# Performance work log

Measured on AMD Instinct MI355X. Metric: run time of the kernel, lower is better.

## Reference

```python
import jax, jax.numpy as jnp
import numpy as np
import math

N, E, T, H, IN_DIM, G, L = 8192, 131072, 262144, 128, 64, 32, 2
RBF_BINS, RBF_MAX, ANG_BINS = 32, 5.0, 16


def _rbf(d, r_max, n_bins):
    centers = jnp.linspace(0.0, r_max, n_bins, dtype=jnp.float32)
    delta = r_max / max(n_bins - 1, 1)
    gamma = 1.0 / (2.0 * (delta ** 2 + 1e-12))
    diff = d[:, None] - centers[None, :]
    return jnp.exp(-gamma * diff * diff)


def _mlp2(x, w1, b1, w2, b2):
    return jax.nn.silu(x @ w1 + b1) @ w2 + b2


def _ln(x, g, b):
    mu = jnp.mean(x, -1, keepdims=True)
    var = jnp.mean((x - mu) ** 2, -1, keepdims=True)
    return (x - mu) * jax.lax.rsqrt(var + 1e-5) * g + b


def _safe_norm(v):
    # ||v|| with grad-safe sqrt at v=0
    return jnp.sqrt(jnp.sum(v * v, -1) + 1e-12)


def setup_inputs() -> dict:
    key = jax.random.key(0)
    ks = iter(jax.random.split(key, 64))

    def lin(fan_in, shape):
        return jax.random.normal(next(ks), shape, jnp.float32) * (fan_in ** -0.5)

    x = jax.random.normal(next(ks), (N, IN_DIM), jnp.float32)
    pos = jax.random.normal(next(ks), (N, 3), jnp.float32) * 2.0
    edge_index = jax.random.randint(next(ks), (2, E), 0, N, jnp.int32)
    edge_dist = jnp.linalg.norm(pos[edge_index[1]] - pos[edge_index[0]], axis=-1)
    triplet_kj = jax.random.randint(next(ks), (T,), 0, E, jnp.int32)
    triplet_ji = jax.random.randint(next(ks), (T,), 0, E, jnp.int32)
    batch = jnp.sort(jax.random.randint(next(ks), (N,), 0, G, jnp.int32))
    TM_IN, MM_IN, CTX = 2 * RBF_BINS + ANG_BINS, 3 * H + RBF_BINS, 3 * H
    d = dict(
        x=x, pos=pos, edge_dist=edge_dist,
        node_in_w=lin(IN_DIM, (IN_DIM, H)), node_in_b=jnp.zeros(H),
        tm_w1=lin(TM_IN, (L, TM_IN, H)), tm_b1=jnp.zeros((L, H)),
        tm_w2=lin(H, (L, H, H)), tm_b2=jnp.zeros((L, H)),
        mm_w1=lin(MM_IN, (L, MM_IN, H)), mm_b1=jnp.zeros((L, H)),
        mm_w2=lin(H, (L, H, 2 * H)), mm_b2=jnp.zeros((L, 2 * H)),
        us_w1=lin(CTX, (L, CTX, H)), us_b1=jnp.zeros((L, H)),
        us_w2=lin(H, (L, H, H)), us_b2=jnp.zeros((L, H)),
        gv_w1=lin(CTX, (L, CTX, H)), gv_b1=jnp.zeros((L, H)),
        gv_w2=lin(H, (L, H, H)), gv_b2=jnp.zeros((L, H)),
        ln_g=jnp.ones((L, H)), ln_b=jnp.zeros((L, H)),
        vn_init=jnp.zeros(H),
        v2n_w1=lin(H, (H, H)), v2n_b1=jnp.zeros(H),
        v2n_w2=lin(H, (H, H)), v2n_b2=jnp.zeros(H),
        n2v_w1=lin(H, (H, H)), n2v_b1=jnp.zeros(H),
        n2v_w2=lin(H, (H, H)), n2v_b2=jnp.zeros(H),
        head_w1=lin(5 * H, (5 * H, H)), head_b1=jnp.zeros(H),
        head_w2=lin(H, (H, 1)), head_b2=jnp.zeros(1),
        edge_index=edge_index, triplet_kj=triplet_kj,
        triplet_ji=triplet_ji, batch=batch,
    )
    return d


def reference(x, pos, edge_dist, node_in_w, node_in_b, tm_w1, tm_b1, tm_w2, tm_b2,
              mm_w1, mm_b1, mm_w2, mm_b2, us_w1, us_b1, us_w2, us_b2,
              gv_w1, gv_b1, gv_w2, gv_b2, ln_g, ln_b, vn_init,
              v2n_w1, v2n_b1, v2n_w2, v2n_b2, n2v_w1, n2v_b1, n2v_w2, n2v_b2,
              head_w1, head_b1, head_w2, head_b2,
              edge_index, triplet_kj, triplet_ji, batch):
    src, dst = edge_index[0], edge_index[1]
    s = x @ node_in_w + node_in_b                              # [N,H]
    v = jnp.zeros((N, H, 3), s.dtype)                          # [N,H,3]
    vec = pos[dst] - pos[src]                                  # [E,3]
    edge_dir = vec / (edge_dist[:, None] + 1e-9)               # [E,3]
    edge_rbf = _rbf(edge_dist, RBF_MAX, RBF_BINS)              # [E,32]
    # 3-body angles between edge ji and edge kj
    a, b = vec[triplet_ji], vec[triplet_kj]                    # [T,3]
    cos = jnp.sum(a * b, -1) / (_safe_norm(a) * _safe_norm(b) + 1e-9)
    angle = jnp.arccos(jnp.clip(cos, -1.0 + 1e-7, 1.0 - 1e-7))
    angle_feat = _rbf(angle, math.pi, ANG_BINS)                # [T,16]
    vn = jnp.broadcast_to(vn_init, (G, H))
    for l in range(L):
        s = s + _mlp2(vn, v2n_w1, v2n_b1, v2n_w2, v2n_b2)[batch]
        # triplet gather -> MLP -> scatter onto edges
        t_in = jnp.concatenate([edge_rbf[triplet_kj], edge_rbf[triplet_ji], angle_feat], -1)
        t_msg = _mlp2(t_in, tm_w1[l], tm_b1[l], tm_w2[l], tm_b2[l])
        angle_agg = jax.ops.segment_sum(t_msg, triplet_ji, num_segments=E)   # [E,H]
        # edge messages -> scatter onto nodes (scalar + vector channels)
        msg_in = jnp.concatenate([s[src], s[dst], edge_rbf, angle_agg], -1)  # [E,416]
        msg = _mlp2(msg_in, mm_w1[l], mm_b1[l], mm_w2[l], mm_b2[l])          # [E,2H]
        m_s, m_vc = msg[:, :H], msg[:, H:]
        agg_s = jax.ops.segment_sum(m_s, dst, num_segments=N)                # [N,H]
        m_v = m_vc[:, :, None] * edge_dir[:, None, :]                        # [E,H,3]
        agg_v = jax.ops.segment_sum(m_v.reshape(E, H * 3), dst, num_segments=N).reshape(N, H, 3)
        ctx = jnp.concatenate([s, agg_s, _safe_norm(v)], -1)                 # [N,3H]
        s = s + _mlp2(ctx, us_w1[l], us_b1[l], us_w2[l], us_b2[l])
        gate = jax.nn.sigmoid(_mlp2(ctx, gv_w1[l], gv_b1[l], gv_w2[l], gv_b2[l]))
        v = v + gate[:, :, None] * agg_v
        s = jax.nn.silu(_ln(s, ln_g[l], ln_b[l]))
        vn = vn + _mlp2(jax.ops.segment_sum(s, batch, num_segments=G),
                        n2v_w1, n2v_b1, n2v_w2, n2v_b2)
    nf = jnp.concatenate([s, _safe_norm(v)], -1)                             # [N,2H]
    add_p = jax.ops.segment_sum(nf, batch, num_segments=G)
    counts = jax.ops.segment_sum(jnp.ones((N,), nf.dtype), batch, num_segments=G)
    mean_p = add_p / jnp.maximum(counts, 1.0)[:, None]
    g = jnp.concatenate([add_p, mean_p, vn], -1)                             # [G,5H]
    pred = _mlp2(g, head_w1, head_b1, head_w2, head_b2)                      # [G,1]
    return pred[:, 0]
```

## Files before the change

kernel.cpp:

```cpp
#include <hip/hip_runtime.h>
#include <math.h>

#define N_   8192
#define E_   131072
#define T_   262144
#define H_   128
#define IND_ 64
#define G_   32
#define L_   2

#define CW 64
#define RB 16

#define MROWS 32
#define HSTRIDE 136
#define WSTRIDE 36

#define STEP_E  ((float)(5.0/31.0))
#define GAMMA_E ((float)(1.0/(2.0*((5.0/31.0)*(5.0/31.0) + 1e-12))))
#define PI_D    3.14159265358979323846
#define STEP_A  ((float)(PI_D/15.0))
#define GAMMA_A ((float)(1.0/(2.0*((PI_D/15.0)*(PI_D/15.0) + 1e-12))))

typedef __attribute__((ext_vector_type(8))) short short8;
typedef __attribute__((ext_vector_type(4))) float f32x4;
typedef unsigned short ushort_t;

static __device__ __forceinline__ float silu_f(float x){ return x / (1.f + expf(-x)); }
static __device__ __forceinline__ float sigmoid_f(float x){ return 1.f / (1.f + expf(-x)); }

static __device__ __forceinline__ ushort_t f2bf(float x){
  unsigned int u = __builtin_bit_cast(unsigned int, x);
  u += 0x7FFFu + ((u >> 16) & 1u);
  return (ushort_t)(u >> 16);
}
static __device__ __forceinline__ float bf2f(ushort_t h){
  unsigned int u = ((unsigned int)h) << 16;
  return __builtin_bit_cast(float, u);
}


__global__ void k_zero(float* __restrict__ p, long n){
  long stride = (long)gridDim.x*256;
  long n4 = n >> 2;
  float4* p4 = (float4*)p;
  for (long i = (long)blockIdx.x*256 + threadIdx.x; i < n4; i += stride)
    p4[i] = make_float4(0.f,0.f,0.f,0.f);
  for (long i = (n4<<2) + (long)blockIdx.x*256 + threadIdx.x; i < n; i += stride)
    p[i] = 0.f;
}

__global__ void k_sentinel(float* __restrict__ p, int n){
  int i = blockIdx.x*256 + threadIdx.x;
  if (i < n) p[i] = 1.0e30f;
}

__global__ void k_init_vn(float* __restrict__ vn, const float* __restrict__ vn_init){
  int i = blockIdx.x*256 + threadIdx.x;
  if (i < G_*H_) vn[i] = vn_init[i & 127];
}

__global__ void k_bhist(const int* __restrict__ batch, int* __restrict__ bh){
  int i = blockIdx.x*256 + threadIdx.x;
  if (i < N_) atomicAdd(&bh[batch[i]], 1);
}
__global__ void k_bscan(int* __restrict__ bh){
  if (threadIdx.x == 0 && blockIdx.x == 0){
    int a = 0;
    for (int g=0; g<G_; g++){ a += bh[g]; bh[g] = a; }
  }
}

__global__ void k_wt_all(const float* __restrict__ tm_w1, const float* __restrict__ tm_w2,
                         const float* __restrict__ mm_w1, const float* __restrict__ mm_w2,
                         const float* __restrict__ us_w1, const float* __restrict__ us_w2,
                         const float* __restrict__ gv_w1, const float* __restrict__ gv_w2,
                         ushort_t* __restrict__ wtbuf){
  const int l = blockIdx.y;
  int i = blockIdx.x*256 + threadIdx.x;
  if (i >= 245760) return;
  ushort_t* base = wtbuf + (size_t)l*376832;
  if (i < 12288){
    int c = i/96, k = i%96;
    base[i] = (k < 80) ? f2bf(tm_w1[(size_t)l*10240 + (size_t)k*128 + c]) : (ushort_t)0;
  } else if (i < 28672){
    int j = i - 12288; int c = j >> 7, k = j & 127;
    base[12288 + j] = f2bf(tm_w2[(size_t)l*16384 + (size_t)k*128 + c]);
  } else if (i < 81920){
    int j = i - 28672; int c = j/416, k = j%416;
    base[28672 + j] = f2bf(mm_w1[(size_t)l*53248 + (size_t)k*128 + c]);
  } else if (i < 114688){
    int j = i - 81920; int c = j >> 7, k = j & 127;
    base[81920 + j] = f2bf(mm_w2[(size_t)l*32768 + (size_t)k*256 + c]);
  } else if (i < 163840){
    int j = i - 114688; int c = j/384, k = j%384;
    float w = us_w1[(size_t)l*49152 + (size_t)k*128 + c];
    ushort_t h = f2bf(w);
    base[114688 + j] = h; base[163840 + j] = f2bf(w - bf2f(h));
  } else if (i < 180224){
    int j = i - 163840; int c = j >> 7, k = j & 127;
    float w = us_w2[(size_t)l*16384 + (size_t)k*128 + c];
    ushort_t h = f2bf(w);
    base[212992 + j] = h; base[229376 + j] = f2bf(w - bf2f(h));
  } else if (i < 229376){
    int j = i - 180224; int c = j/384, k = j%384;
    float w = gv_w1[(size_t)l*49152 + (size_t)k*128 + c];
    ushort_t h = f2bf(w);
    base[245760 + j] = h; base[294912 + j] = f2bf(w - bf2f(h));
  } else {
    int j = i - 229376; int c = j >> 7, k = j & 127;
    float w = gv_w2[(size_t)l*16384 + (size_t)k*128 + c];
    ushort_t h = f2bf(w);
    base[344064 + j] = h; base[360448 + j] = f2bf(w - bf2f(h));
  }
}

__global__ void k_geom(const float* __restrict__ pos, const float* __restrict__ dist,
                       const int* __restrict__ ei,
                       float* __restrict__ vec, float* __restrict__ dir,
                       ushort_t* __restrict__ rbf16){
  int e = blockIdx.x*256 + threadIdx.x;
  if (e >= E_) return;
  int s = ei[e], d = ei[E_ + e];
  float vx = pos[d*3+0] - pos[s*3+0];
  float vy = pos[d*3+1] - pos[s*3+1];
  float vz = pos[d*3+2] - pos[s*3+2];
  vec[e*3+0]=vx; vec[e*3+1]=vy; vec[e*3+2]=vz;
  float dd = dist[e];
  float inv = 1.f / (dd + 1e-9f);
  dir[e*3+0]=vx*inv; dir[e*3+1]=vy*inv; dir[e*3+2]=vz*inv;
  #pragma unroll
  for (int i=0;i<32;i++){
    float df = dd - i*STEP_E;
    rbf16[e*32+i] = f2bf(expf(-GAMMA_E*df*df));
  }
}

__global__ void k_dirs(const float* __restrict__ dir, const int* __restrict__ perm_e,
                       float* __restrict__ dir_s){
  int p = blockIdx.x*256 + threadIdx.x;
  if (p >= E_) return;
  int e = perm_e[p];
  dir_s[p*3+0] = dir[e*3+0];
  dir_s[p*3+1] = dir[e*3+1];
  dir_s[p*3+2] = dir[e*3+2];
}

__global__ void k_angle(const float* __restrict__ vec,
                        const int* __restrict__ kj, const int* __restrict__ ji,
                        float* __restrict__ angle){
  int t = blockIdx.x*256 + threadIdx.x;
  if (t >= T_) return;
  int ea = ji[t], eb = kj[t];
  float ax=vec[ea*3+0], ay=vec[ea*3+1], az=vec[ea*3+2];
  float bx=vec[eb*3+0], by=vec[eb*3+1], bz=vec[eb*3+2];
  float dot = ax*bx + ay*by + az*bz;
  float na = sqrtf(ax*ax+ay*ay+az*az + 1e-12f);
  float nb = sqrtf(bx*bx+by*by+bz*bz + 1e-12f);
  float c = dot / (na*nb + 1e-9f);
  c = fminf(fmaxf(c, -1.f + 1e-7f), 1.f - 1e-7f);
  angle[t] = acosf(c);
}


__global__ void k_hist(const int* __restrict__ keys, int M, int* __restrict__ hist){
  int i = blockIdx.x*256 + threadIdx.x;
  if (i < M) atomicAdd(&hist[keys[i]], 1);
}

__global__ void k_hist2(const int* __restrict__ keys, const int* __restrict__ map,
                        int M, int* __restrict__ hist){
  int i = blockIdx.x*256 + threadIdx.x;
  if (i < M) atomicAdd(&hist[map[keys[i]]], 1);
}

__global__ void k_scan1(const int* __restrict__ in, int* __restrict__ out,
                        int* __restrict__ sums, int B){
  __shared__ int sh[1024];
  int base = blockIdx.x*1024, t = threadIdx.x;
  for (int j=t;j<1024;j+=256) sh[j] = (base+j<B) ? in[base+j] : 0;
  __syncthreads();
  for (int o=1;o<1024;o<<=1){
    int v[4];
    #pragma unroll
    for (int q=0;q<4;q++){ int idx=t+q*256; v[q]=(idx>=o)? sh[idx-o]:0; }
    __syncthreads();
    #pragma unroll
    for (int q=0;q<4;q++){ int idx=t+q*256; sh[idx]+=v[q]; }
    __syncthreads();
  }
  for (int j=t;j<1024;j+=256) if (base+j<B) out[base+j] = (j==0)?0:sh[j-1];
  if (t==0) sums[blockIdx.x] = sh[1023];
}

__global__ void k_scan2(int* __restrict__ sums, int nb){
  if (threadIdx.x==0 && blockIdx.x==0){
    int a=0;
    for (int i=0;i<nb;i++){ int x=sums[i]; sums[i]=a; a+=x; }
  }
}

__global__ void k_scan3(int* __restrict__ out, const int* __restrict__ sums, int B){
  int i = blockIdx.x*256+threadIdx.x;
  if (i<B) out[i] += sums[i>>10];
}

__global__ void k_fill(const int* __restrict__ keys, int M, int* __restrict__ cur,
                       int* __restrict__ perm){
  int i = blockIdx.x*256+threadIdx.x;
  if (i<M){ int p = atomicAdd(&cur[keys[i]],1); perm[p]=i; }
}

__global__ void k_fill2(const int* __restrict__ keys, const int* __restrict__ map,
                        int M, int* __restrict__ cur, int* __restrict__ perm){
  int i = blockIdx.x*256+threadIdx.x;
  if (i<M){ int p = atomicAdd(&cur[map[keys[i]]],1); perm[p]=i; }
}

__global__ void k_invert(const int* __restrict__ perm, int* __restrict__ rank, int M){
  int i = blockIdx.x*256+threadIdx.x;
  if (i<M) rank[perm[i]] = i;
}

template<int SM, int K1PAD>
__launch_bounds__(256, 3)
__global__ void k_mlp1(
    const int* __restrict__ perm,
    const int* __restrict__ idx1, const int* __restrict__ idx2,
    const ushort_t* __restrict__ rbf16, const float* __restrict__ angle,
    const ushort_t* __restrict__ s16, const ushort_t* __restrict__ eagg_in,
    const ushort_t* __restrict__ W1t, const float* __restrict__ b1,
    ushort_t* __restrict__ outbuf)
{
  __shared__ ushort_t lw[128*WSTRIDE];
  __shared__ ushort_t hid[4*MROWS*HSTRIDE];
  const int tid  = threadIdx.x;
  const int wave = tid >> 6;
  const int lane = tid & 63;
  const int n    = lane & 15;
  const int quad = lane >> 4;
  const int kq   = quad*8;
  const int wrow = blockIdx.x*128 + wave*MROWS;
  ushort_t* myhid = hid + wave*MROWS*HSTRIDE;

  const int e0 = perm[wrow + n];
  const int e1 = perm[wrow + 16 + n];

  int i1a = idx1[e0], i1b = idx1[e1];
  int i2a = idx2[e0], i2b = idx2[e1];
  float ang0 = 0.f, ang1 = 0.f;
  if (SM == 1){ ang0 = angle[e0]; ang1 = angle[e1]; }

  f32x4 acc[2][8];
  #pragma unroll
  for (int rh=0;rh<2;rh++)
    #pragma unroll
    for (int ct=0;ct<8;ct++) acc[rh][ct] = (f32x4){0.f,0.f,0.f,0.f};

  #pragma unroll
  for (int k0 = 0; k0 < K1PAD; k0 += 32){
    #pragma unroll
    for (int it=0; it<2; it++){
      int idx = tid + it*256;
      int col = idx >> 2, seg = idx & 3;
      *(short8*)&lw[col*WSTRIDE + seg*8] = *(const short8*)&W1t[(size_t)col*K1PAD + k0 + seg*8];
    }
    __syncthreads();

    short8 a0, a1;
    if (SM == 1){
      if (k0 == 0){
        a0 = *(const short8*)&rbf16[(size_t)i1a*32 + kq];
        a1 = *(const short8*)&rbf16[(size_t)i1b*32 + kq];
      } else if (k0 == 32){
        a0 = *(const short8*)&rbf16[(size_t)i2a*32 + kq];
        a1 = *(const short8*)&rbf16[(size_t)i2b*32 + kq];
      } else {
        #pragma unroll
        for (int j=0;j<8;j++){
          int kk = kq + j;
          float v0 = 0.f, v1 = 0.f;
          if (kk < 16){
            float c = (float)kk*STEP_A;
            float d0 = ang0 - c, d1 = ang1 - c;
            v0 = expf(-GAMMA_A*d0*d0); v1 = expf(-GAMMA_A*d1*d1);
          }
          a0[j] = (short)f2bf(v0); a1[j] = (short)f2bf(v1);
        }
      }
    } else {
      const int k = k0 + kq;
      if (k0 < 128){
        a0 = *(const short8*)&s16[(size_t)i1a*128 + k];
        a1 = *(const short8*)&s16[(size_t)i1b*128 + k];
      } else if (k0 < 256){
        a0 = *(const short8*)&s16[(size_t)i2a*128 + (k-128)];
        a1 = *(const short8*)&s16[(size_t)i2b*128 + (k-128)];
      } else if (k0 < 288){
        a0 = *(const short8*)&rbf16[(size_t)e0*32 + (k-256)];
        a1 = *(const short8*)&rbf16[(size_t)e1*32 + (k-256)];
      } else {
        a0 = *(const short8*)&eagg_in[(size_t)(wrow + n)*128 + (k-288)];
        a1 = *(const short8*)&eagg_in[(size_t)(wrow + 16 + n)*128 + (k-288)];
      }
    }
    #pragma unroll
    for (int ct=0;ct<8;ct++){
      short8 b = *(const short8*)&lw[(ct*16 + n)*WSTRIDE + kq];
      acc[0][ct] = __builtin_amdgcn_mfma_f32_16x16x32_bf16(a0, b, acc[0][ct], 0,0,0);
      acc[1][ct] = __builtin_amdgcn_mfma_f32_16x16x32_bf16(a1, b, acc[1][ct], 0,0,0);
    }
    __syncthreads();
  }

  #pragma unroll
  for (int rh=0;rh<2;rh++){
    #pragma unroll
    for (int ct=0;ct<8;ct++){
      int col = ct*16 + n;
      float bv = b1[col];
      #pragma unroll
      for (int reg=0;reg<4;reg++){
        int rloc = rh*16 + quad*4 + reg;
        float h = acc[rh][ct][reg] + bv;
        myhid[rloc*HSTRIDE + col] = f2bf(silu_f(h));
      }
    }
  }
  const int rsub = lane >> 4;
  const int c8   = (lane & 15) * 8;
  #pragma unroll
  for (int i=0;i<8;i++){
    int rloc = i*4 + rsub;
    int grow = wrow + rloc;
    short8 vv = *(const short8*)&myhid[(size_t)rloc*HSTRIDE + c8];
    *(short8*)&outbuf[(size_t)grow*128 + c8] = vv;
  }
}

__launch_bounds__(64, 4)
__global__ void k_aggemm_t(const ushort_t* __restrict__ tmsg, const int* __restrict__ tends,
                           const ushort_t* __restrict__ W2t, const float* __restrict__ b2,
                           ushort_t* __restrict__ eagg2){
  __shared__ ushort_t hid[MROWS*HSTRIDE];
  const int lane = threadIdx.x;
  const int n    = lane & 15;
  const int quad = lane >> 4;
  const int kq   = quad*8;
  const int wrow = blockIdx.x*MROWS;
  const int r0 = wrow + n, r1 = wrow + 16 + n;
  const int s0 = r0 ? tends[r0-1] : 0;
  const int e0 = tends[r0];
  const int s1 = tends[r1-1];
  const int e1 = tends[r1];

  f32x4 acc[2][8];
  #pragma unroll
  for (int rh=0;rh<2;rh++)
    #pragma unroll
    for (int ct=0;ct<8;ct++) acc[rh][ct] = (f32x4){0.f,0.f,0.f,0.f};

  #pragma unroll
  for (int k0=0;k0<128;k0+=32){
    float sum0[8], sum1[8];
    #pragma unroll
    for (int j=0;j<8;j++){ sum0[j]=0.f; sum1[j]=0.f; }
    for (int p=s0;p<e0;p++){
      short8 w = *(const short8*)&tmsg[(size_t)p*128 + k0 + kq];
      #pragma unroll
      for (int j=0;j<8;j++) sum0[j] += bf2f((ushort_t)w[j]);
    }
    for (int p=s1;p<e1;p++){
      short8 w = *(const short8*)&tmsg[(size_t)p*128 + k0 + kq];
      #pragma unroll
      for (int j=0;j<8;j++) sum1[j] += bf2f((ushort_t)w[j]);
    }
    short8 a0, a1;
    #pragma unroll
    for (int j=0;j<8;j++){
      a0[j] = (short)f2bf(sum0[j]);
      a1[j] = (short)f2bf(sum1[j]);
    }
    #pragma unroll
    for (int ct=0;ct<8;ct++){
      short8 b = *(const short8*)&W2t[(size_t)(ct*16 + n)*128 + k0 + kq];
      acc[0][ct] = __builtin_amdgcn_mfma_f32_16x16x32_bf16(a0, b, acc[0][ct], 0,0,0);
      acc[1][ct] = __builtin_amdgcn_mfma_f32_16x16x32_bf16(a1, b, acc[1][ct], 0,0,0);
    }
  }

  float cnts[2][4];
  #pragma unroll
  for (int rh=0;rh<2;rh++)
    #pragma unroll
    for (int reg=0;reg<4;reg++){
      int row = wrow + rh*16 + quad*4 + reg;
      cnts[rh][reg] = (float)(tends[row] - (row ? tends[row-1] : 0));
    }

  #pragma unroll
  for (int rh=0;rh<2;rh++){
    #pragma unroll
    for (int ct=0;ct<8;ct++){
      int col = ct*16 + n;
      float bv = b2[col];
      #pragma unroll
      for (int reg=0;reg<4;reg++){
        int rloc = rh*16 + quad*4 + reg;
        hid[rloc*HSTRIDE + col] = f2bf(acc[rh][ct][reg] + cnts[rh][reg]*bv);
      }
    }
  }
  const int rsub = lane >> 4;
  const int c8   = (lane & 15) * 8;
  #pragma unroll
  for (int i=0;i<8;i++){
    int rloc = i*4 + rsub;
    int grow = wrow + rloc;
    short8 vv = *(const short8*)&hid[(size_t)rloc*HSTRIDE + c8];
    *(short8*)&eagg2[(size_t)grow*128 + c8] = vv;
  }
}

__global__ void k_agg_e(const ushort_t* __restrict__ hbuf, const int* __restrict__ eends,
                        const float* __restrict__ dir_s, float* __restrict__ mom){
  int i = blockIdx.x*256 + threadIdx.x;
  int d = i >> 6, c2 = (i & 63)*2;
  if (d >= N_) return;
  int s = (d == 0) ? 0 : eends[d-1];
  int e = eends[d];
  float hs0=0.f,hs1=0.f, hx0=0.f,hx1=0.f, hy0=0.f,hy1=0.f, hz0=0.f,hz1=0.f;
  float sdx=0.f, sdy=0.f, sdz=0.f;
  for (int q=s;q<e;q++){
    unsigned int w = *(const unsigned int*)&hbuf[(size_t)q*128 + c2];
    float h0 = bf2f((ushort_t)(w & 0xFFFFu));
    float h1 = bf2f((ushort_t)(w >> 16));
    float dx = dir_s[q*3+0], dy = dir_s[q*3+1], dz = dir_s[q*3+2];
    hs0 += h0; hs1 += h1;
    hx0 += h0*dx; hx1 += h1*dx;
    hy0 += h0*dy; hy1 += h1*dy;
    hz0 += h0*dz; hz1 += h1*dz;
    sdx += dx; sdy += dy; sdz += dz;
  }
  size_t base = (size_t)d*128 + c2;
  *(float2*)&mom[base]                        = make_float2(hs0, hs1);
  *(float2*)&mom[(size_t)N_*128   + base]     = make_float2(hx0, hx1);
  *(float2*)&mom[(size_t)N_*256   + base]     = make_float2(hy0, hy1);
  *(float2*)&mom[(size_t)N_*384   + base]     = make_float2(hz0, hz1);
  if (c2 == 0){
    mom[(size_t)N_*512 + d*4+0] = sdx;
    mom[(size_t)N_*512 + d*4+1] = sdy;
    mom[(size_t)N_*512 + d*4+2] = sdz;
  }
}

__launch_bounds__(64, 4)
__global__ void k_gemm_e(const float* __restrict__ mom, const int* __restrict__ eends,
                         const ushort_t* __restrict__ W2t ,
                         const float* __restrict__ b2 ,
                         const float* __restrict__ v ,
                         ushort_t* __restrict__ a16h, ushort_t* __restrict__ a16l,
                         ushort_t* __restrict__ vnh,  ushort_t* __restrict__ vnl,
                         float* __restrict__ aggv ){
  __shared__ float sbuf[MROWS*130];
  const int lane = threadIdx.x;
  const int n    = lane & 15;
  const int quad = lane >> 4;
  const int kq   = quad*8;
  const int wrow = blockIdx.x*MROWS;
  const int og   = blockIdx.y;

  const float* M = mom + (size_t)og*((size_t)N_*128);
  const ushort_t* W = W2t + (og ? (size_t)128*128 : 0);

  f32x4 acc[2][8];
  #pragma unroll
  for (int rh=0;rh<2;rh++)
    #pragma unroll
    for (int ct=0;ct<8;ct++) acc[rh][ct] = (f32x4){0.f,0.f,0.f,0.f};

  #pragma unroll
  for (int k0=0;k0<128;k0+=32){
    const int k = k0 + kq;
    const float* p0 = &M[(size_t)(wrow + n)*128 + k];
    const float* p1 = &M[(size_t)(wrow + 16 + n)*128 + k];
    f32x4 x0 = *(const f32x4*)p0, x1 = *(const f32x4*)(p0+4);
    f32x4 y0 = *(const f32x4*)p1, y1 = *(const f32x4*)(p1+4);
    short8 ah0, al0, ah1, al1;
    #pragma unroll
    for (int j=0;j<4;j++){
      ushort_t h;
      h = f2bf(x0[j]); ah0[j]   = (short)h; al0[j]   = (short)f2bf(x0[j] - bf2f(h));
      h = f2bf(x1[j]); ah0[4+j] = (short)h; al0[4+j] = (short)f2bf(x1[j] - bf2f(h));
      h = f2bf(y0[j]); ah1[j]   = (short)h; al1[j]   = (short)f2bf(y0[j] - bf2f(h));
      h = f2bf(y1[j]); ah1[4+j] = (short)h; al1[4+j] = (short)f2bf(y1[j] - bf2f(h));
    }
    #pragma unroll
    for (int ct=0;ct<8;ct++){
      short8 b = *(const short8*)&W[(size_t)(ct*16 + n)*128 + k0 + kq];
      acc[0][ct] = __builtin_amdgcn_mfma_f32_16x16x32_bf16(ah0, b, acc[0][ct], 0,0,0);
      acc[0][ct] = __builtin_amdgcn_mfma_f32_16x16x32_bf16(al0, b, acc[0][ct], 0,0,0);
      acc[1][ct] = __builtin_amdgcn_mfma_f32_16x16x32_bf16(ah1, b, acc[1][ct], 0,0,0);
      acc[1][ct] = __builtin_amdgcn_mfma_f32_16x16x32_bf16(al1, b, acc[1][ct], 0,0,0);
    }
  }

  const int rsub = lane >> 4;
  const int c8   = (lane & 15) * 8;

  if (og == 0){
    float cnts[2][4];
    #pragma unroll
    for (int rh=0;rh<2;rh++)
      #pragma unroll
      for (int reg=0;reg<4;reg++){
        int row = wrow + rh*16 + quad*4 + reg;
        cnts[rh][reg] = (float)(eends[row] - (row ? eends[row-1] : 0));
      }
    ushort_t* us = (ushort_t*)sbuf;
    #pragma unroll
    for (int rh=0;rh<2;rh++)
      #pragma unroll
      for (int ct=0;ct<8;ct++){
        int col = ct*16 + n;
        float bv = b2[col];
        #pragma unroll
        for (int reg=0;reg<4;reg++){
          int rloc = rh*16 + quad*4 + reg;
          float val = acc[rh][ct][reg] + cnts[rh][reg]*bv;
          us[rloc*HSTRIDE + col] = f2bf(val);
        }
      }
    #pragma unroll
    for (int i=0;i<8;i++){
      int rloc = i*4 + rsub;
      short8 vv = *(const short8*)&us[(size_t)rloc*HSTRIDE + c8];
      *(short8*)&a16h[(size_t)(wrow + rloc)*128 + c8] = vv;
    }
    #pragma unroll
    for (int rh=0;rh<2;rh++)
      #pragma unroll
      for (int ct=0;ct<8;ct++){
        int col = ct*16 + n;
        float bv = b2[col];
        #pragma unroll
        for (int reg=0;reg<4;reg++){
          int rloc = rh*16 + quad*4 + reg;
          float val = acc[rh][ct][reg] + cnts[rh][reg]*bv;
          ushort_t h = f2bf(val);
          us[rloc*HSTRIDE + col] = f2bf(val - bf2f(h));
        }
      }
    #pragma unroll
    for (int i=0;i<8;i++){
      int rloc = i*4 + rsub;
      short8 vv = *(const short8*)&us[(size_t)rloc*HSTRIDE + c8];
      *(short8*)&a16l[(size_t)(wrow + rloc)*128 + c8] = vv;
    }
    #pragma unroll 4
    for (int j=0;j<32;j++){
      size_t idx = (size_t)wrow*128 + (size_t)j*128 + lane*2;
      float2 a = *(const float2*)&v[idx];
      float2 b = *(const float2*)&v[(size_t)N_*128 + idx];
      float2 c = *(const float2*)&v[(size_t)N_*256 + idx];
      float n0 = sqrtf(a.x*a.x + b.x*b.x + c.x*c.x + 1e-12f);
      float n1 = sqrtf(a.y*a.y + b.y*b.y + c.y*c.y + 1e-12f);
      ushort_t h0 = f2bf(n0), h1 = f2bf(n1);
      *(unsigned int*)&vnh[idx] = (unsigned int)h0 | ((unsigned int)h1 << 16);
      *(unsigned int*)&vnl[idx] = (unsigned int)f2bf(n0 - bf2f(h0))
                                | ((unsigned int)f2bf(n1 - bf2f(h1)) << 16);
    }
  } else {
    const int x = og - 1;
    #pragma unroll
    for (int rh=0;rh<2;rh++)
      #pragma unroll
      for (int ct=0;ct<8;ct++){
        int col = ct*16 + n;
        float bv = b2[128 + col];
        #pragma unroll
        for (int reg=0;reg<4;reg++){
          int rloc = rh*16 + quad*4 + reg;
          int row = wrow + rloc;
          float sd = mom[(size_t)N_*512 + row*4 + x];
          sbuf[rloc*130 + col] = acc[rh][ct][reg] + sd*bv;
        }
      }
    float* plane = aggv + (size_t)x*((size_t)N_*128);
    #pragma unroll
    for (int i=0;i<8;i++){
      int rloc = i*4 + rsub;
      f32x4 v0 = *(const f32x4*)&sbuf[rloc*130 + c8];
      f32x4 v1 = *(const f32x4*)&sbuf[rloc*130 + c8 + 4];
      *(f32x4*)&plane[(size_t)(wrow + rloc)*128 + c8] = v0;
      *(f32x4*)&plane[(size_t)(wrow + rloc)*128 + c8 + 4] = v1;
    }
  }
}

__launch_bounds__(256, 3)
__global__ void k_node_mfma(
    const float* __restrict__ s_in,
    const ushort_t* __restrict__ a16h, const ushort_t* __restrict__ a16l,
    const ushort_t* __restrict__ vnh,  const ushort_t* __restrict__ vnl,
    float* __restrict__ s2, float* __restrict__ v_out ,
    const float* __restrict__ aggv ,
    const ushort_t* __restrict__ us1h, const ushort_t* __restrict__ us1l, const float* __restrict__ us_b1,
    const ushort_t* __restrict__ us2h, const ushort_t* __restrict__ us2l, const float* __restrict__ us_b2,
    const ushort_t* __restrict__ gv1h, const ushort_t* __restrict__ gv1l, const float* __restrict__ gv_b1,
    const ushort_t* __restrict__ gv2h, const ushort_t* __restrict__ gv2l, const float* __restrict__ gv_b2)
{
  __shared__ ushort_t lwh[128*WSTRIDE];
  __shared__ ushort_t lwl[128*WSTRIDE];
  __shared__ ushort_t hidh[4][16*HSTRIDE];
  __shared__ ushort_t hidl[4][16*HSTRIDE];
  const int tid  = threadIdx.x;
  const int wave = tid >> 6;
  const int lane = tid & 63;
  const int n    = lane & 15;
  const int quad = lane >> 4;
  const int kq   = quad*8;
  const int og   = blockIdx.y;
  const int wrow = blockIdx.x*64 + wave*16;
  const int r0 = wrow + n;

  const ushort_t* W1h = og ? gv1h : us1h;
  const ushort_t* W1l = og ? gv1l : us1l;
  const float*    B1  = og ? gv_b1 : us_b1;
  const ushort_t* W2h = og ? gv2h : us2h;
  const ushort_t* W2l = og ? gv2l : us2l;
  const float*    B2  = og ? gv_b2 : us_b2;

  f32x4 acc[8];
  #pragma unroll
  for (int ct=0;ct<8;ct++) acc[ct] = (f32x4){0.f,0.f,0.f,0.f};

  #pragma unroll
  for (int k0=0; k0<384; k0+=32){
    #pragma unroll
    for (int it = 0; it < 2; it++){
      int idx = tid + it*256;
      int col = idx >> 2, seg = idx & 3;
      *(short8*)&lwh[col*WSTRIDE + seg*8] = *(const short8*)&W1h[(size_t)col*384 + k0 + seg*8];
      *(short8*)&lwl[col*WSTRIDE + seg*8] = *(const short8*)&W1l[(size_t)col*384 + k0 + seg*8];
    }
    __syncthreads();

    short8 ah0, al0;
    const int k = k0 + kq;
    if (k0 < 128){
      const float* p0 = &s_in[(size_t)r0*128 + k];
      f32x4 x0 = *(const f32x4*)p0, x1 = *(const f32x4*)(p0+4);
      #pragma unroll
      for (int j=0;j<4;j++){
        ushort_t h;
        h = f2bf(x0[j]); ah0[j]   = (short)h; al0[j]   = (short)f2bf(x0[j] - bf2f(h));
        h = f2bf(x1[j]); ah0[4+j] = (short)h; al0[4+j] = (short)f2bf(x1[j] - bf2f(h));
      }
    } else if (k0 < 256){
      int kk = k - 128;
      ah0 = *(const short8*)&a16h[(size_t)r0*128 + kk];
      al0 = *(const short8*)&a16l[(size_t)r0*128 + kk];
    } else {
      int kk = k - 256;
      ah0 = *(const short8*)&vnh[(size_t)r0*128 + kk];
      al0 = *(const short8*)&vnl[(size_t)r0*128 + kk];
    }
    #pragma unroll
    for (int ct=0;ct<8;ct++){
      short8 bh = *(const short8*)&lwh[(ct*16 + n)*WSTRIDE + kq];
      short8 bl = *(const short8*)&lwl[(ct*16 + n)*WSTRIDE + kq];
      acc[ct] = __builtin_amdgcn_mfma_f32_16x16x32_bf16(ah0, bh, acc[ct], 0,0,0);
      acc[ct] = __builtin_amdgcn_mfma_f32_16x16x32_bf16(al0, bh, acc[ct], 0,0,0);
      acc[ct] = __builtin_amdgcn_mfma_f32_16x16x32_bf16(ah0, bl, acc[ct], 0,0,0);
    }
    __syncthreads();
  }

  #pragma unroll
  for (int ct=0;ct<8;ct++){
    int col = ct*16 + n;
    float bv = B1[col];
    #pragma unroll
    for (int reg=0;reg<4;reg++){
      int rloc = quad*4 + reg;
      float h = silu_f(acc[ct][reg] + bv);
      ushort_t hh = f2bf(h);
      hidh[wave][rloc*HSTRIDE + col] = hh;
      hidl[wave][rloc*HSTRIDE + col] = f2bf(h - bf2f(hh));
    }
  }

  f32x4 acc2[8];
  #pragma unroll
  for (int ct=0;ct<8;ct++) acc2[ct] = (f32x4){0.f,0.f,0.f,0.f};

  #pragma unroll
  for (int k0=0;k0<128;k0+=32){
    #pragma unroll
    for (int it = 0; it < 2; it++){
      int idx = tid + it*256;
      int col = idx >> 2, seg = idx & 3;
      *(short8*)&lwh[col*WSTRIDE + seg*8] = *(const short8*)&W2h[(size_t)col*128 + k0 + seg*8];
      *(short8*)&lwl[col*WSTRIDE + seg*8] = *(const short8*)&W2l[(size_t)col*128 + k0 + seg*8];
    }
    __syncthreads();

    short8 ah0 = *(const short8*)&hidh[wave][(size_t)(n)*HSTRIDE + k0 + kq];
    short8 al0 = *(const short8*)&hidl[wave][(size_t)(n)*HSTRIDE + k0 + kq];
    #pragma unroll
    for (int ct=0;ct<8;ct++){
      short8 bh = *(const short8*)&lwh[(ct*16 + n)*WSTRIDE + kq];
      short8 bl = *(const short8*)&lwl[(ct*16 + n)*WSTRIDE + kq];
      acc2[ct] = __builtin_amdgcn_mfma_f32_16x16x32_bf16(ah0, bh, acc2[ct], 0,0,0);
      acc2[ct] = __builtin_amdgcn_mfma_f32_16x16x32_bf16(al0, bh, acc2[ct], 0,0,0);
      acc2[ct] = __builtin_amdgcn_mfma_f32_16x16x32_bf16(ah0, bl, acc2[ct], 0,0,0);
    }
    __syncthreads();
  }

  if (og == 0){
    #pragma unroll
    for (int ct=0;ct<8;ct++){
      int col = ct*16 + n;
      float bv = B2[col];
      #pragma unroll
      for (int reg=0;reg<4;reg++){
        int row = wrow + quad*4 + reg;
        size_t idx = (size_t)row*128 + col;
        s2[idx] = s_in[idx] + acc2[ct][reg] + bv;
      }
    }
  } else {
    #pragma unroll
    for (int ct=0;ct<8;ct++){
      int col = ct*16 + n;
      float bv = B2[col];
      #pragma unroll
      for (int reg=0;reg<4;reg++){
        int row = wrow + quad*4 + reg;
        size_t idx = (size_t)row*128 + col;
        float g = sigmoid_f(acc2[ct][reg] + bv);
        v_out[idx]                    += g*aggv[idx];
        v_out[(size_t)N_*128 + idx]   += g*aggv[(size_t)N_*128 + idx];
        v_out[(size_t)N_*256 + idx]   += g*aggv[(size_t)N_*256 + idx];
      }
    }
  }
}

__launch_bounds__(128)
__global__ void k_gemm(const float* __restrict__ A,
                       const float* __restrict__ W,
                       const float* __restrict__ bias,
                       float* __restrict__ C, int R, int K)
{
  __shared__ float ws[CW*128];
  __shared__ float as[RB][CW];
  const int tid = threadIdx.x;
  const int nchunk = (K + CW - 1) / CW;

  for (int rb = blockIdx.x*RB; rb < R; rb += gridDim.x*RB){
    float acc[RB];
    #pragma unroll
    for (int r=0;r<RB;r++) acc[r] = 0.f;

    for (int c=0;c<nchunk;c++){
      const int k0 = c*CW;
      for (int i=tid; i<CW*128; i+=128){
        int kk = i >> 7, col = i & 127;
        int k = k0 + kk;
        ws[i] = (k < K) ? W[k*128 + col] : 0.f;
      }
      for (int i=tid; i<RB*CW; i+=128){
        int r  = i >> 6, kk = i & 63;
        int k  = k0 + kk;
        as[r][kk] = (k < K) ? A[(long)(rb+r)*K + k] : 0.f;
      }
      __syncthreads();
      #pragma unroll 4
      for (int kq2=0; kq2<CW/4; kq2++){
        float w0 = ws[(4*kq2+0)*128 + tid];
        float w1 = ws[(4*kq2+1)*128 + tid];
        float w2 = ws[(4*kq2+2)*128 + tid];
        float w3 = ws[(4*kq2+3)*128 + tid];
        #pragma unroll
        for (int r=0;r<RB;r++){
          const float4 av = *reinterpret_cast<const float4*>(&as[r][4*kq2]);
          acc[r] = fmaf(av.x, w0, acc[r]);
          acc[r] = fmaf(av.y, w1, acc[r]);
          acc[r] = fmaf(av.z, w2, acc[r]);
          acc[r] = fmaf(av.w, w3, acc[r]);
        }
      }
      __syncthreads();
    }

    const float bv = bias[tid];
    #pragma unroll
    for (int r=0;r<RB;r++)
      C[(long)(rb+r)*128 + tid] = acc[r] + bv;
  }
}


__launch_bounds__(256)
__global__ void k_small_mlp2(const float* __restrict__ in,
                             const float* __restrict__ w1, const float* __restrict__ b1,
                             const float* __restrict__ w2, const float* __restrict__ b2,
                             float* __restrict__ outp, int accumulate){
  __shared__ float a[4][128];
  __shared__ float h[4][128];
  int tid = threadIdx.x;
  int rbase = blockIdx.x*4;
  for (int i=tid;i<4*128;i+=256) a[i>>7][i&127] = in[(rbase + (i>>7))*128 + (i&127)];
  __syncthreads();
  int col = tid & 127, rg = tid >> 7;
  float acc0=0.f, acc1=0.f;
  for (int k=0;k<128;k++){
    float w = w1[k*128+col];
    acc0 = fmaf(a[rg*2+0][k], w, acc0);
    acc1 = fmaf(a[rg*2+1][k], w, acc1);
  }
  {
    float bv = b1[col];
    h[rg*2+0][col] = silu_f(acc0+bv);
    h[rg*2+1][col] = silu_f(acc1+bv);
  }
  __syncthreads();
  acc0=0.f; acc1=0.f;
  for (int k=0;k<128;k++){
    float w = w2[k*128+col];
    acc0 = fmaf(h[rg*2+0][k], w, acc0);
    acc1 = fmaf(h[rg*2+1][k], w, acc1);
  }
  {
    float bv = b2[col];
    int idx0 = (rbase+rg*2+0)*128+col;
    int idx1 = (rbase+rg*2+1)*128+col;
    float v0 = acc0+bv, v1 = acc1+bv;
    outp[idx0] = accumulate ? outp[idx0]+v0 : v0;
    outp[idx1] = accumulate ? outp[idx1]+v1 : v1;
  }
}

__global__ void k_head(const float* __restrict__ gbuf,
                       const float* __restrict__ w1, const float* __restrict__ b1,
                       const float* __restrict__ w2, const float* __restrict__ b2,
                       float* __restrict__ outp){
  __shared__ float red[128];
  int g = blockIdx.x, tid = threadIdx.x;
  float acc = 0.f;
  for (int k=0;k<640;k++) acc = fmaf(gbuf[g*640+k], w1[k*128+tid], acc);
  float h = silu_f(acc + b1[tid]);
  red[tid] = h * w2[tid];
  __syncthreads();
  for (int o=64;o>0;o>>=1){ if (tid<o) red[tid]+=red[tid+o]; __syncthreads(); }
  if (tid == 0) outp[g] = red[0] + b2[0];
}


__global__ void k_sadd_batch(float* __restrict__ s, const float* __restrict__ t2,
                             const int* __restrict__ batch, ushort_t* __restrict__ s16){
  int i = blockIdx.x*256 + threadIdx.x;
  if (i >= N_*H_) return;
  int n = i >> 7, h = i & 127;
  float v = s[i] + t2[batch[n]*128 + h];
  s[i] = v;
  s16[i] = f2bf(v);
}

__global__ void k_ln_silu(const float* __restrict__ in, float* __restrict__ outp,
                          const float* __restrict__ g, const float* __restrict__ b){
  __shared__ float red[128];
  int n = blockIdx.x, tid = threadIdx.x;
  float x = in[n*128 + tid];
  red[tid] = x; __syncthreads();
  for (int o=64;o>0;o>>=1){ if (tid<o) red[tid]+=red[tid+o]; __syncthreads(); }
  float mu = red[0] * (1.f/128.f);
  __syncthreads();
  float dx = x - mu;
  red[tid] = dx*dx; __syncthreads();
  for (int o=64;o>0;o>>=1){ if (tid<o) red[tid]+=red[tid+o]; __syncthreads(); }
  float var = red[0] * (1.f/128.f);
  float y = dx * rsqrtf(var + 1e-5f) * g[tid] + b[tid];
  outp[n*128 + tid] = silu_f(y);
}

__global__ void k_ssum_csr(const float* __restrict__ s, const int* __restrict__ bends,
                           float* __restrict__ ssum){
  int g = blockIdx.x, c = blockIdx.y, tid = threadIdx.x;
  int s0 = g ? bends[g-1] : 0;
  int e0 = bends[g];
  long len = e0 - s0;
  int lo = s0 + (int)((len*c) >> 3);
  int hi = s0 + (int)((len*(c+1)) >> 3);
  float a = 0.f;
  for (int n=lo; n<hi; n++) a += s[(size_t)n*128 + tid];
  if (hi > lo) atomicAdd(&ssum[g*128 + tid], a);
}

__global__ void k_scatter_nf2(const float* __restrict__ s, const float* __restrict__ v ,
                              const int* __restrict__ batch, float* __restrict__ addp){
  int j = threadIdx.x;
  int base = blockIdx.x*32;
  float acc = 0.f;
  int prev = batch[base];
  for (int r=0;r<32;r++){
    int nn = base + r;
    int b = batch[nn];
    if (b != prev){ atomicAdd(&addp[prev*256 + j], acc); acc = 0.f; prev = b; }
    float val;
    if (j < 128){
      val = s[(size_t)nn*128 + j];
    } else {
      size_t idx = (size_t)nn*128 + (j - 128);
      float v0 = v[idx], v1 = v[(size_t)N_*128 + idx], v2 = v[(size_t)N_*256 + idx];
      val = sqrtf(v0*v0 + v1*v1 + v2*v2 + 1e-12f);
    }
    acc += val;
  }
  atomicAdd(&addp[prev*256 + j], acc);
}

__global__ void k_build_g(const float* __restrict__ addp, const int* __restrict__ bends,
                          const float* __restrict__ vn, float* __restrict__ gbuf){
  int i = blockIdx.x*256 + threadIdx.x;
  if (i >= G_*640) return;
  int g = i / 640, j = i % 640;
  float cnt = (float)(bends[g] - (g ? bends[g-1] : 0));
  float val;
  if (j < 256)       val = addp[g*256 + j];
  else if (j < 512)  val = addp[g*256 + (j-256)] / fmaxf(cnt, 1.f);
  else               val = vn[g*128 + (j-512)];
  gbuf[i] = val;
}


extern "C" void kernel_launch(void* const* d_in, const int* in_sizes, int n_in,
                              void* d_out, int out_size, void* d_ws, size_t ws_size,
                              hipStream_t stream)
{
  const float* x         = (const float*)d_in[0];
  const float* pos       = (const float*)d_in[1];
  const float* edist     = (const float*)d_in[2];
  const float* node_in_w = (const float*)d_in[3];
  const float* node_in_b = (const float*)d_in[4];
  const float* tm_w1 = (const float*)d_in[5];
  const float* tm_b1 = (const float*)d_in[6];
  const float* tm_w2 = (const float*)d_in[7];
  const float* tm_b2 = (const float*)d_in[8];
  const float* mm_w1 = (const float*)d_in[9];
  const float* mm_b1 = (const float*)d_in[10];
  const float* mm_w2 = (const float*)d_in[11];
  const float* mm_b2 = (const float*)d_in[12];
  const float* us_w1 = (const float*)d_in[13];
  const float* us_b1 = (const float*)d_in[14];
  const float* us_w2 = (const float*)d_in[15];
  const float* us_b2 = (const float*)d_in[16];
  const float* gv_w1 = (const float*)d_in[17];
  const float* gv_b1 = (const float*)d_in[18];
  const float* gv_w2 = (const float*)d_in[19];
  const float* gv_b2 = (const float*)d_in[20];
  const float* ln_g  = (const float*)d_in[21];
  const float* ln_b  = (const float*)d_in[22];
  const float* vn_init = (const float*)d_in[23];
  const float* v2n_w1 = (const float*)d_in[24];
  const float* v2n_b1 = (const float*)d_in[25];
  const float* v2n_w2 = (const float*)d_in[26];
  const float* v2n_b2 = (const float*)d_in[27];
  const float* n2v_w1 = (const float*)d_in[28];
  const float* n2v_b1 = (const float*)d_in[29];
  const float* n2v_w2 = (const float*)d_in[30];
  const float* n2v_b2 = (const float*)d_in[31];
  const float* head_w1 = (const float*)d_in[32];
  const float* head_b1 = (const float*)d_in[33];
  const float* head_w2 = (const float*)d_in[34];
  const float* head_b2 = (const float*)d_in[35];
  const int* ei    = (const int*)d_in[36];
  const int* t_kj  = (const int*)d_in[37];
  const int* t_ji  = (const int*)d_in[38];
  const int* batch = (const int*)d_in[39];
  float* out = (float*)d_out;

  float* f = (float*)d_ws;
  size_t off = 0;
  auto alloc = [&](size_t n){ n = (n + 3) & ~(size_t)3; float* p = f + off; off += n; return p; };
  float*    vec    = alloc((size_t)E_*3);
  float*    dir    = alloc((size_t)E_*3);
  ushort_t* rbf16  = (ushort_t*)alloc((size_t)E_*16);
  float*    angle  = alloc((size_t)T_);
  float*    tmsg_f = alloc((size_t)E_*128);
  float*    eagg2_f= alloc((size_t)E_*64);
  float*    dir_s  = alloc((size_t)E_*3);
  float*    tends_f= alloc((size_t)E_ + 1024);
  float*    eends_f= alloc((size_t)N_ + 1024);
  float*    bends_f= alloc((size_t)G_);
  float*    s      = alloc((size_t)N_*128);
  ushort_t* s16    = (ushort_t*)alloc((size_t)N_*64);
  float*    v      = alloc((size_t)N_*384);
  float*    aggv   = alloc((size_t)N_*384);
  float*    rank_f = alloc((size_t)E_);
  float*    wtbuf_f= alloc((size_t)376832);
  float*    vn     = alloc((size_t)G_*128);
  float*    tg2    = alloc((size_t)G_*128);
  float*    ssum   = alloc((size_t)G_*128);
  float*    addp   = alloc((size_t)G_*256);
  float*    gbuf   = alloc((size_t)G_*640);

  if (off * sizeof(float) > ws_size){
    k_sentinel<<<1, 64, 0, stream>>>(out, G_);
    return;
  }

  int* perm_t = (int*)vec;
  int* perm_e = perm_t + T_;
  int* rank_e = (int*)rank_f;
  int* tends  = (int*)tends_f;
  int* eends  = (int*)eends_f;
  int* bends  = (int*)bends_f;
  ushort_t* tmsg   = (ushort_t*)tmsg_f;
  ushort_t* ehid   = (ushort_t*)tmsg_f;
  ushort_t* eagg2  = (ushort_t*)eagg2_f;
  float*    mom  = eagg2_f;
  ushort_t* a16h = (ushort_t*)(eagg2_f + 4227072);
  ushort_t* a16l = a16h + (size_t)N_*128;
  ushort_t* vnh  = a16l + (size_t)N_*128;
  ushort_t* vnl  = vnh  + (size_t)N_*128;
  float*    s2   = (float*)(vnl + (size_t)N_*128);

  ushort_t* wtbuf = (ushort_t*)wtbuf_f;
  auto WT = [&](int l, size_t o){ return wtbuf + (size_t)l*376832 + o; };

  auto zero = [&](float* p, long n){
    int blocks = (int)((n/4 + 255)/256); if (blocks > 16384) blocks = 16384; if (blocks < 1) blocks = 1;
    k_zero<<<blocks, 256, 0, stream>>>(p, n);
  };
  auto csort = [&](const int* keys, const int* map, int M, int B, int* perm, int* ends){
    int nb = (B+1023)/1024;
    zero((float*)ends, B + nb);
    if (map) k_hist2<<<(M+255)/256, 256, 0, stream>>>(keys, map, M, ends);
    else     k_hist <<<(M+255)/256, 256, 0, stream>>>(keys, M, ends);
    k_scan1<<<nb, 256, 0, stream>>>(ends, ends, ends + B, B);
    k_scan2<<<1, 64, 0, stream>>>(ends + B, nb);
    k_scan3<<<(B+255)/256, 256, 0, stream>>>(ends, ends + B, B);
    if (map) k_fill2<<<(M+255)/256, 256, 0, stream>>>(keys, map, M, ends, perm);
    else     k_fill <<<(M+255)/256, 256, 0, stream>>>(keys, M, ends, perm);
  };

  zero(v, (long)N_*384);
  k_init_vn<<<(G_*H_ + 255)/256, 256, 0, stream>>>(vn, vn_init);
  k_geom<<<(E_ + 255)/256, 256, 0, stream>>>(pos, edist, ei, vec, dir, rbf16);
  k_angle<<<(T_ + 255)/256, 256, 0, stream>>>(vec, t_kj, t_ji, angle);
  csort(ei+E_, nullptr, E_, N_, perm_e, eends);
  k_invert<<<(E_+255)/256, 256, 0, stream>>>(perm_e, rank_e, E_);
  k_dirs<<<(E_+255)/256, 256, 0, stream>>>(dir, perm_e, dir_s);
  csort(t_ji, rank_e, T_, E_, perm_t, tends);
  zero(bends_f, G_);
  k_bhist<<<(N_+255)/256, 256, 0, stream>>>(batch, bends);
  k_bscan<<<1, 64, 0, stream>>>(bends);
  k_wt_all<<<dim3(960, 2), 256, 0, stream>>>(tm_w1, tm_w2, mm_w1, mm_w2,
                                             us_w1, us_w2, gv_w1, gv_w2, wtbuf);
  k_gemm<<<512, 128, 0, stream>>>(x, node_in_w, node_in_b, s, N_, IND_);

  for (int l=0; l<L_; l++){
    k_small_mlp2<<<8, 256, 0, stream>>>(vn, v2n_w1, v2n_b1, v2n_w2, v2n_b2, tg2, 0);
    k_sadd_batch<<<(N_*H_ + 255)/256, 256, 0, stream>>>(s, tg2, batch, s16);

    k_mlp1<1,96><<<T_/128, 256, 0, stream>>>(perm_t, t_kj, t_ji,
        rbf16, angle, s16, eagg2, WT(l,0), tm_b1 + l*128, tmsg);
    k_aggemm_t<<<E_/MROWS, 64, 0, stream>>>(tmsg, tends, WT(l,12288), tm_b2 + l*128, eagg2);

    k_mlp1<2,416><<<E_/128, 256, 0, stream>>>(perm_e, ei, ei + E_,
        rbf16, angle, s16, eagg2, WT(l,28672), mm_b1 + l*128, ehid);
    k_agg_e<<<(N_*64)/256, 256, 0, stream>>>(ehid, eends, dir_s, mom);
    k_gemm_e<<<dim3(N_/MROWS, 4), 64, 0, stream>>>(mom, eends, WT(l,81920), mm_b2 + l*256,
        v, a16h, a16l, vnh, vnl, aggv);

    k_node_mfma<<<dim3(N_/64, 2), 256, 0, stream>>>(s, a16h, a16l, vnh, vnl, s2, v, aggv,
        WT(l,114688), WT(l,163840), us_b1 + l*128, WT(l,212992), WT(l,229376), us_b2 + l*128,
        WT(l,245760), WT(l,294912), gv_b1 + l*128, WT(l,344064), WT(l,360448), gv_b2 + l*128);

    k_ln_silu<<<N_, 128, 0, stream>>>(s2, s, ln_g + l*128, ln_b + l*128);
    zero(ssum, (long)G_*128);
    k_ssum_csr<<<dim3(G_, 8), 128, 0, stream>>>(s, bends, ssum);
    k_small_mlp2<<<8, 256, 0, stream>>>(ssum, n2v_w1, n2v_b1, n2v_w2, n2v_b2, vn, 1);
  }

  zero(addp, (long)G_*256);
  k_scatter_nf2<<<N_/32, 256, 0, stream>>>(s, v, batch, addp);
  k_build_g<<<(G_*640 + 255)/256, 256, 0, stream>>>(addp, bends, vn, gbuf);
  k_head<<<G_, 128, 0, stream>>>(gbuf, head_w1, head_b1, head_w2, head_b2, out);
}
```

Measured before the change: 866.1 us.

## Drop LDS weight staging in k_mlp1, use single-wave blocks with prefetched gathers

Rewrites k_mlp1 as one 64-thread wave per block with no __syncthreads. B-fragments of the weight matrix are read straight from global memory instead of being staged in LDS, and all gathered A-fragments (rbf, angle basis, node states) are prefetched into registers before the MFMA loop. The goal is to remove barrier stalls and expose gather latency earlier. In exchange, each wave re-reads weights through the cache, uses more registers, and loses cross-wave sharing of weight tiles.

```diff
diff --git a/kernel.cpp b/kernel.cpp
--- a/kernel.cpp
+++ b/kernel.cpp
@@ -223,7 +223,7 @@
 }
 
 template<int SM, int K1PAD>
-__launch_bounds__(256, 3)
+__launch_bounds__(64, 2)
 __global__ void k_mlp1(
     const int* __restrict__ perm,
     const int* __restrict__ idx1, const int* __restrict__ idx2,
@@ -232,24 +232,52 @@
     const ushort_t* __restrict__ W1t, const float* __restrict__ b1,
     ushort_t* __restrict__ outbuf)
 {
-  __shared__ ushort_t lw[128*WSTRIDE];
-  __shared__ ushort_t hid[4*MROWS*HSTRIDE];
-  const int tid  = threadIdx.x;
-  const int wave = tid >> 6;
-  const int lane = tid & 63;
+  __shared__ ushort_t hid[MROWS*HSTRIDE];
+  const int lane = threadIdx.x;
   const int n    = lane & 15;
   const int quad = lane >> 4;
   const int kq   = quad*8;
-  const int wrow = blockIdx.x*128 + wave*MROWS;
-  ushort_t* myhid = hid + wave*MROWS*HSTRIDE;
+  const int wrow = blockIdx.x*MROWS;
 
   const int e0 = perm[wrow + n];
   const int e1 = perm[wrow + 16 + n];
 
   int i1a = idx1[e0], i1b = idx1[e1];
   int i2a = idx2[e0], i2b = idx2[e1];
-  float ang0 = 0.f, ang1 = 0.f;
-  if (SM == 1){ ang0 = angle[e0]; ang1 = angle[e1]; }
+
+  constexpr int NPF = (SM==1) ? 3 : 9;
+  short8 pa[NPF], pb[NPF];
+  if (SM == 1){
+    pa[0] = *(const short8*)&rbf16[(size_t)i1a*32 + kq];
+    pb[0] = *(const short8*)&rbf16[(size_t)i1b*32 + kq];
+    pa[1] = *(const short8*)&rbf16[(size_t)i2a*32 + kq];
+    pb[1] = *(const short8*)&rbf16[(size_t)i2b*32 + kq];
+    float ang0 = angle[e0], ang1 = angle[e1];
+    #pragma unroll
+    for (int j=0;j<8;j++){
+      int kk = kq + j;
+      float v0 = 0.f, v1 = 0.f;
+      if (kk < 16){
+        float c = (float)kk*STEP_A;
+        float d0 = ang0 - c, d1 = ang1 - c;
+        v0 = expf(-GAMMA_A*d0*d0); v1 = expf(-GAMMA_A*d1*d1);
+      }
+      pa[2][j] = (short)f2bf(v0); pb[2][j] = (short)f2bf(v1);
+    }
+  } else {
+    #pragma unroll
+    for (int c=0;c<4;c++){
+      pa[c] = *(const short8*)&s16[(size_t)i1a*128 + c*32 + kq];
+      pb[c] = *(const short8*)&s16[(size_t)i1b*128 + c*32 + kq];
+    }
+    #pragma unroll
+    for (int c=4;c<8;c++){
+      pa[c] = *(const short8*)&s16[(size_t)i2a*128 + (c-4)*32 + kq];
+      pb[c] = *(const short8*)&s16[(size_t)i2b*128 + (c-4)*32 + kq];
+    }
+    pa[8] = *(const short8*)&rbf16[(size_t)e0*32 + kq];
+    pb[8] = *(const short8*)&rbf16[(size_t)e1*32 + kq];
+  }
 
   f32x4 acc[2][8];
   #pragma unroll
@@ -259,58 +287,21 @@
 
   #pragma unroll
   for (int k0 = 0; k0 < K1PAD; k0 += 32){
-    #pragma unroll
-    for (int it=0; it<2; it++){
-      int idx = tid + it*256;
-      int col = idx >> 2, seg = idx & 3;
-      *(short8*)&lw[col*WSTRIDE + seg*8] = *(const short8*)&W1t[(size_t)col*K1PAD + k0 + seg*8];
-    }
-    __syncthreads();
-
+    constexpr int dummy = 0; (void)dummy;
+    const int c = k0 >> 5;
     short8 a0, a1;
-    if (SM == 1){
-      if (k0 == 0){
-        a0 = *(const short8*)&rbf16[(size_t)i1a*32 + kq];
-        a1 = *(const short8*)&rbf16[(size_t)i1b*32 + kq];
-      } else if (k0 == 32){
-        a0 = *(const short8*)&rbf16[(size_t)i2a*32 + kq];
-        a1 = *(const short8*)&rbf16[(size_t)i2b*32 + kq];
-      } else {
-        #pragma unroll
-        for (int j=0;j<8;j++){
-          int kk = kq + j;
-          float v0 = 0.f, v1 = 0.f;
-          if (kk < 16){
-            float c = (float)kk*STEP_A;
-            float d0 = ang0 - c, d1 = ang1 - c;
-            v0 = expf(-GAMMA_A*d0*d0); v1 = expf(-GAMMA_A*d1*d1);
-          }
-          a0[j] = (short)f2bf(v0); a1[j] = (short)f2bf(v1);
-        }
-      }
+    if (c < NPF){
+      a0 = pa[c]; a1 = pb[c];
     } else {
-      const int k = k0 + kq;
-      if (k0 < 128){
-        a0 = *(const short8*)&s16[(size_t)i1a*128 + k];
-        a1 = *(const short8*)&s16[(size_t)i1b*128 + k];
-      } else if (k0 < 256){
-        a0 = *(const short8*)&s16[(size_t)i2a*128 + (k-128)];
-        a1 = *(const short8*)&s16[(size_t)i2b*128 + (k-128)];
-      } else if (k0 < 288){
-        a0 = *(const short8*)&rbf16[(size_t)e0*32 + (k-256)];
-        a1 = *(const short8*)&rbf16[(size_t)e1*32 + (k-256)];
-      } else {
-        a0 = *(const short8*)&eagg_in[(size_t)(wrow + n)*128 + (k-288)];
-        a1 = *(const short8*)&eagg_in[(size_t)(wrow + 16 + n)*128 + (k-288)];
-      }
+      a0 = *(const short8*)&eagg_in[(size_t)(wrow + n)*128 + (k0 - 288) + kq];
+      a1 = *(const short8*)&eagg_in[(size_t)(wrow + 16 + n)*128 + (k0 - 288) + kq];
     }
     #pragma unroll
     for (int ct=0;ct<8;ct++){
-      short8 b = *(const short8*)&lw[(ct*16 + n)*WSTRIDE + kq];
+      short8 b = *(const short8*)&W1t[(size_t)(ct*16 + n)*K1PAD + k0 + kq];
       acc[0][ct] = __builtin_amdgcn_mfma_f32_16x16x32_bf16(a0, b, acc[0][ct], 0,0,0);
       acc[1][ct] = __builtin_amdgcn_mfma_f32_16x16x32_bf16(a1, b, acc[1][ct], 0,0,0);
     }
-    __syncthreads();
   }
 
   #pragma unroll
@@ -323,7 +314,7 @@
       for (int reg=0;reg<4;reg++){
         int rloc = rh*16 + quad*4 + reg;
         float h = acc[rh][ct][reg] + bv;
-        myhid[rloc*HSTRIDE + col] = f2bf(silu_f(h));
+        hid[rloc*HSTRIDE + col] = f2bf(silu_f(h));
       }
     }
   }
@@ -333,7 +324,7 @@
   for (int i=0;i<8;i++){
     int rloc = i*4 + rsub;
     int grow = wrow + rloc;
-    short8 vv = *(const short8*)&myhid[(size_t)rloc*HSTRIDE + c8];
+    short8 vv = *(const short8*)&hid[(size_t)rloc*HSTRIDE + c8];
     *(short8*)&outbuf[(size_t)grow*128 + c8] = vv;
   }
 }
@@ -1067,11 +1058,11 @@
     k_small_mlp2<<<8, 256, 0, stream>>>(vn, v2n_w1, v2n_b1, v2n_w2, v2n_b2, tg2, 0);
     k_sadd_batch<<<(N_*H_ + 255)/256, 256, 0, stream>>>(s, tg2, batch, s16);
 
-    k_mlp1<1,96><<<T_/128, 256, 0, stream>>>(perm_t, t_kj, t_ji,
+    k_mlp1<1,96><<<T_/MROWS, 64, 0, stream>>>(perm_t, t_kj, t_ji,
         rbf16, angle, s16, eagg2, WT(l,0), tm_b1 + l*128, tmsg);
     k_aggemm_t<<<E_/MROWS, 64, 0, stream>>>(tmsg, tends, WT(l,12288), tm_b2 + l*128, eagg2);
 
-    k_mlp1<2,416><<<E_/128, 256, 0, stream>>>(perm_e, ei, ei + E_,
+    k_mlp1<2,416><<<E_/MROWS, 64, 0, stream>>>(perm_e, ei, ei + E_,
         rbf16, angle, s16, eagg2, WT(l,28672), mm_b1 + l*128, ehid);
     k_agg_e<<<(N_*64)/256, 256, 0, stream>>>(ehid, eends, dir_s, mom);
     k_gemm_e<<<dim3(N_/MROWS, 4), 64, 0, stream>>>(mom, eends, WT(l,81920), mm_b2 + l*256,
```

Result: no change. 882.6 us (+1.9%).
